# Kernel tuning notes

Hardware: AMD Instinct MI355X
Metric: run time of the kernel (lower is better)

Reference implementation:

```python
import jax, jax.numpy as jnp
import numpy as np

B, P, O, D, K, NREG, H, NLAYERS = 2, 2048, 512, 256, 3, 2, 8, 2
EPS_COS = 1e-8
EPS_LN = 1e-5


def setup_inputs() -> dict:
    key = jax.random.key(0)
    k = jax.random.split(key, 8)
    s = 0.02
    return {
        "x_path": jax.random.normal(k[0], (B, P, D), jnp.float32),
        "x_omic": jax.random.normal(k[1], (B, O, D), jnp.float32),
        "bottle_tokens": jax.random.uniform(k[2], (1, NREG, D), jnp.float32),
        "Wlp": jax.random.normal(k[3], (D, D), jnp.float32) * s,
        "blp": jnp.zeros((D,), jnp.float32),
        "Wlo": jax.random.normal(k[4], (D, D), jnp.float32) * s,
        "blo": jnp.zeros((D,), jnp.float32),
        "ln_g": jnp.ones((NLAYERS, D), jnp.float32),
        "ln_b": jnp.zeros((NLAYERS, D), jnp.float32),
        "Wqkv": jax.random.normal(k[5], (NLAYERS, D, 3 * D), jnp.float32) * s,
        "bqkv": jnp.zeros((NLAYERS, 3 * D), jnp.float32),
        "Wo": jax.random.normal(k[6], (NLAYERS, D, D), jnp.float32) * s,
        "bo": jnp.zeros((NLAYERS, D), jnp.float32),
    }


def _cosine_sim(xp, xo):
    # xp: [P, D], xo: [O, D] -> [P, O]; torch cosine_similarity semantics
    np_ = jnp.maximum(jnp.linalg.norm(xp, axis=-1), EPS_COS)
    no_ = jnp.maximum(jnp.linalg.norm(xo, axis=-1), EPS_COS)
    return (xp @ xo.T) / (np_[:, None] * no_[None, :])


def _greedy_pairs(sim):
    # exclusive greedy top-K matching == iterative argmax with row/col masking
    Pn, On = sim.shape

    def step(carry, _):
        rm, cm = carry
        masked = jnp.where(rm[:, None] | cm[None, :], -jnp.inf, sim)
        idx = jnp.argmax(masked)
        ip, io = idx // On, idx % On
        return (rm.at[ip].set(True), cm.at[io].set(True)), (ip, io)

    (rm, cm), (ips, ios) = jax.lax.scan(
        step, (jnp.zeros(Pn, bool), jnp.zeros(On, bool)), None, length=K)
    return ips, ios, rm, cm


def _remaining(x, mask, n_keep):
    # non-selected tokens in ascending original order (stable argsort)
    order = jnp.argsort(mask.astype(jnp.int32))
    return x[order[:n_keep]]


def _assemble_one(xp, xo, bottle, Wlp, blp, Wlo, blo):
    sim = _cosine_sim(xp, xo)  # indices are data-dependent but non-differentiable
    ips, ios, rm, cm = _greedy_pairs(sim)
    ks = (xp[ips] @ Wlp + blp) + (xo[ios] @ Wlo + blo)  # [K, D], in greedy order
    rem_p = _remaining(xp, rm, P - K)  # [P-K, D]
    rem_o = _remaining(xo, cm, O - K)  # [O-K, D]
    return jnp.concatenate([ks, rem_p, bottle, rem_o], axis=0)  # [L, D]


def _layernorm(x, g, b):
    mu = jnp.mean(x, axis=-1, keepdims=True)
    var = jnp.mean(jnp.square(x - mu), axis=-1, keepdims=True)
    return (x - mu) * jax.lax.rsqrt(var + EPS_LN) * g + b


def _mhsa(x, Wqkv, bqkv, Wo, bo):
    Bn, L, Dn = x.shape
    dh = Dn // H
    qkv = x @ Wqkv + bqkv  # [B, L, 3D]
    q, k, v = jnp.split(qkv, 3, axis=-1)
    q = q.reshape(Bn, L, H, dh)
    k = k.reshape(Bn, L, H, dh)
    v = v.reshape(Bn, L, H, dh)
    scores = jnp.einsum('bqhd,bkhd->bhqk', q, k) * (1.0 / np.sqrt(dh)).astype(x.dtype)
    attn = jax.nn.softmax(scores, axis=-1)
    out = jnp.einsum('bhqk,bkhd->bqhd', attn, v).reshape(Bn, L, Dn)
    return out @ Wo + bo


def reference(x_path, x_omic, bottle_tokens, Wlp, blp, Wlo, blo,
              ln_g, ln_b, Wqkv, bqkv, Wo, bo):
    path_len, token_len = P, NREG
    x = jax.vmap(_assemble_one, in_axes=(0, 0, None, None, None, None, None))(
        x_path, x_omic, bottle_tokens[0], Wlp, blp, Wlo, blo)  # [B, L, D]
    for l in range(NLAYERS):  # pre-LN residual attention block (TransLayer)
        x = x + _mhsa(_layernorm(x, ln_g[l], ln_b[l]), Wqkv[l], bqkv[l], Wo[l], bo[l])
    t_path, xp_out = x[:, :1, :], x[:, 1:path_len, :]
    t_omic = x[:, path_len + token_len:path_len + token_len + 1, :]
    xo_out = x[:, path_len + token_len + 1:, :]
    return (t_path, xp_out, t_omic, xo_out)
```

## Files before the change

kernel.cpp:

```cpp
#include <hip/hip_runtime.h>
#include <hip/hip_bf16.h>
#include <math.h>

namespace {
constexpr int Bn = 2, Pn = 2048, On = 512, Dn = 256, Kn = 3, NREG = 2, Hn = 8, NL = 2;
constexpr int Ln = Pn + NREG + On - Kn;
constexpr int Lpad = 2560;
constexpr int DH = 32;
constexpr int BH = Bn * Hn;
constexpr float EPS_COS = 1e-8f, EPS_LN = 1e-5f;
constexpr float QS2 = 0.17677669529663687f * 1.4426950408889634f;

using bf16x8 = __attribute__((ext_vector_type(8))) short;
using f32x4  = __attribute__((ext_vector_type(4))) float;

union U8 { int4 i4; ushort u[8]; short s[8]; bf16x8 b; };
union U4 { uint2 i2; ushort u[4]; };

__device__ inline ushort f2bf(float f) {
  union { __bf16 h; ushort u; } c; c.h = (__bf16)f; return c.u;
}

__device__ inline float fexp2(float x) {
#if __has_builtin(__builtin_amdgcn_exp2f)
  return __builtin_amdgcn_exp2f(x);
#else
  float r;
  asm("v_exp_f32 %0, %1" : "=v"(r) : "v"(x));
  return r;
#endif
}

__device__ inline int kswz(int r) {
  return ((r & 1) | ((r & 4) >> 1) | ((r & 2) << 1)) << 3;
}

template<int C> __device__ inline float dppf(float x) {
  return __builtin_bit_cast(float,
      __builtin_amdgcn_update_dpp(0, __builtin_bit_cast(int, x), C, 0xF, 0xF, false));
}
__device__ inline float red16_sum(float x) {
  x += dppf<0xB1>(x);
  x += dppf<0x4E>(x);
  x += dppf<0x124>(x);
  x += dppf<0x128>(x);
  return x;
}

__global__ void k_rownorm(const float* __restrict__ xp, const float* __restrict__ xo,
                          float* __restrict__ xps, float* __restrict__ xos) {
  int r = blockIdx.x;
  const float* src; float* dst;
  if (r < Bn * Pn) { src = xp + (size_t)r * Dn; dst = xps + (size_t)r * Dn; }
  else { int r2 = r - Bn * Pn; src = xo + (size_t)r2 * Dn; dst = xos + (size_t)r2 * Dn; }
  int tid = threadIdx.x;
  float v = src[tid];
  float ss = v * v;
  #pragma unroll
  for (int m = 32; m >= 1; m >>= 1) ss += __shfl_xor(ss, m, 64);
  __shared__ float wsum[4];
  if ((tid & 63) == 0) wsum[tid >> 6] = ss;
  __syncthreads();
  float tot = wsum[0] + wsum[1] + wsum[2] + wsum[3];
  dst[tid] = v * (1.f / fmaxf(sqrtf(tot), EPS_COS));
}

__global__ void k_transpose(const float* __restrict__ xos, float* __restrict__ xosT) {
  __shared__ float t[16][17];
  int b = blockIdx.z;
  int o0 = blockIdx.x * 16, d0 = blockIdx.y * 16;
  int tx = threadIdx.x & 15, ty = threadIdx.x >> 4;
  t[ty][tx] = xos[((size_t)b * On + o0 + ty) * Dn + d0 + tx];
  __syncthreads();
  xosT[((size_t)b * Dn + d0 + ty) * On + o0 + tx] = t[tx][ty];
}

__global__ void k_wprep(const float* __restrict__ W, ushort* __restrict__ Wt, int Kd, int N) {
  const int z = blockIdx.z;
  const int n0 = blockIdx.x * 16, k0 = blockIdx.y * 16;
  const int tx = threadIdx.x & 15, ty = threadIdx.x >> 4;
  __shared__ float t[16][17];
  t[ty][tx] = W[(size_t)z * Kd * N + (size_t)(k0 + ty) * N + n0 + tx];
  __syncthreads();
  Wt[(size_t)z * Kd * N + (size_t)(n0 + ty) * Kd + k0 + tx] = f2bf(t[tx][ty]);
}

__global__ __launch_bounds__(256) void k_gemm64(
    const float* __restrict__ A, long sA,
    const float* __restrict__ Wm, long sW,
    float* __restrict__ C, long sC,
    int M, int N, int Kd)
{
  const int bz = blockIdx.z;
  A += (size_t)bz * sA; Wm += (size_t)bz * sW; C += (size_t)bz * sC;
  const int bm = blockIdx.x * 64, bn = blockIdx.y * 64;
  __shared__ __attribute__((aligned(16))) float As[64][33];
  __shared__ __attribute__((aligned(16))) float Bs[32][64];
  const int tid = threadIdx.x;
  const int ty = tid >> 4, tx = tid & 15;
  const int arow = tid >> 3, acol = (tid & 7) * 4;
  const int brow = tid >> 4, bcol = (tid & 15) * 4;
  float acc[4][4] = {};
  for (int k0 = 0; k0 < Kd; k0 += 32) {
    __syncthreads();
    #pragma unroll
    for (int pp = 0; pp < 2; ++pp) {
      int r = arow + pp * 32;
      float4 v = *(const float4*)(A + (size_t)(bm + r) * Kd + k0 + acol);
      As[r][acol + 0] = v.x; As[r][acol + 1] = v.y; As[r][acol + 2] = v.z; As[r][acol + 3] = v.w;
      int r2 = brow + pp * 16;
      *(float4*)&Bs[r2][bcol] = *(const float4*)(Wm + (size_t)(k0 + r2) * N + bn + bcol);
    }
    __syncthreads();
    #pragma unroll
    for (int kk = 0; kk < 32; ++kk) {
      float a0 = As[ty * 4 + 0][kk], a1 = As[ty * 4 + 1][kk];
      float a2 = As[ty * 4 + 2][kk], a3 = As[ty * 4 + 3][kk];
      float4 bq = *(const float4*)&Bs[kk][tx * 4];
      acc[0][0] += a0 * bq.x; acc[0][1] += a0 * bq.y; acc[0][2] += a0 * bq.z; acc[0][3] += a0 * bq.w;
      acc[1][0] += a1 * bq.x; acc[1][1] += a1 * bq.y; acc[1][2] += a1 * bq.z; acc[1][3] += a1 * bq.w;
      acc[2][0] += a2 * bq.x; acc[2][1] += a2 * bq.y; acc[2][2] += a2 * bq.z; acc[2][3] += a2 * bq.w;
      acc[3][0] += a3 * bq.x; acc[3][1] += a3 * bq.y; acc[3][2] += a3 * bq.z; acc[3][3] += a3 * bq.w;
    }
  }
  #pragma unroll
  for (int i = 0; i < 4; ++i) {
    int gr = bm + ty * 4 + i;
    *(float4*)(C + (size_t)gr * N + bn + tx * 4) =
        make_float4(acc[i][0], acc[i][1], acc[i][2], acc[i][3]);
  }
}

__global__ __launch_bounds__(64) void k_gemm_qkv(
    const ushort* __restrict__ A, const ushort* __restrict__ Bt,
    const float* __restrict__ bias,
    ushort* __restrict__ Qh, ushort* __restrict__ Kh, ushort* __restrict__ Vtg, int M)
{
  const int m0 = blockIdx.x * 64, n0 = blockIdx.y * 64;
  const int lane = threadIdx.x, lm = lane & 15, lh = lane >> 4;
  f32x4 acc[4][4] = {};
  int rA[4];
  #pragma unroll
  for (int mi = 0; mi < 4; ++mi) { int r = m0 + mi * 16 + lm; rA[mi] = r < M ? r : M - 1; }
  const ushort* bp0 = Bt + (size_t)(n0 +  0 + lm) * 256 + lh * 8;
  const ushort* bp1 = Bt + (size_t)(n0 + 16 + lm) * 256 + lh * 8;
  const ushort* bp2 = Bt + (size_t)(n0 + 32 + lm) * 256 + lh * 8;
  const ushort* bp3 = Bt + (size_t)(n0 + 48 + lm) * 256 + lh * 8;
  #pragma unroll
  for (int k0 = 0; k0 < 256; k0 += 32) {
    U8 a0, a1, a2, a3, b0, b1, b2, b3;
    a0.i4 = *(const int4*)(A + (size_t)rA[0] * 256 + k0 + lh * 8);
    a1.i4 = *(const int4*)(A + (size_t)rA[1] * 256 + k0 + lh * 8);
    a2.i4 = *(const int4*)(A + (size_t)rA[2] * 256 + k0 + lh * 8);
    a3.i4 = *(const int4*)(A + (size_t)rA[3] * 256 + k0 + lh * 8);
    b0.i4 = *(const int4*)(bp0 + k0);
    b1.i4 = *(const int4*)(bp1 + k0);
    b2.i4 = *(const int4*)(bp2 + k0);
    b3.i4 = *(const int4*)(bp3 + k0);
    acc[0][0] = __builtin_amdgcn_mfma_f32_16x16x32_bf16(a0.b, b0.b, acc[0][0], 0, 0, 0);
    acc[0][1] = __builtin_amdgcn_mfma_f32_16x16x32_bf16(a0.b, b1.b, acc[0][1], 0, 0, 0);
    acc[0][2] = __builtin_amdgcn_mfma_f32_16x16x32_bf16(a0.b, b2.b, acc[0][2], 0, 0, 0);
    acc[0][3] = __builtin_amdgcn_mfma_f32_16x16x32_bf16(a0.b, b3.b, acc[0][3], 0, 0, 0);
    acc[1][0] = __builtin_amdgcn_mfma_f32_16x16x32_bf16(a1.b, b0.b, acc[1][0], 0, 0, 0);
    acc[1][1] = __builtin_amdgcn_mfma_f32_16x16x32_bf16(a1.b, b1.b, acc[1][1], 0, 0, 0);
    acc[1][2] = __builtin_amdgcn_mfma_f32_16x16x32_bf16(a1.b, b2.b, acc[1][2], 0, 0, 0);
    acc[1][3] = __builtin_amdgcn_mfma_f32_16x16x32_bf16(a1.b, b3.b, acc[1][3], 0, 0, 0);
    acc[2][0] = __builtin_amdgcn_mfma_f32_16x16x32_bf16(a2.b, b0.b, acc[2][0], 0, 0, 0);
    acc[2][1] = __builtin_amdgcn_mfma_f32_16x16x32_bf16(a2.b, b1.b, acc[2][1], 0, 0, 0);
    acc[2][2] = __builtin_amdgcn_mfma_f32_16x16x32_bf16(a2.b, b2.b, acc[2][2], 0, 0, 0);
    acc[2][3] = __builtin_amdgcn_mfma_f32_16x16x32_bf16(a2.b, b3.b, acc[2][3], 0, 0, 0);
    acc[3][0] = __builtin_amdgcn_mfma_f32_16x16x32_bf16(a3.b, b0.b, acc[3][0], 0, 0, 0);
    acc[3][1] = __builtin_amdgcn_mfma_f32_16x16x32_bf16(a3.b, b1.b, acc[3][1], 0, 0, 0);
    acc[3][2] = __builtin_amdgcn_mfma_f32_16x16x32_bf16(a3.b, b2.b, acc[3][2], 0, 0, 0);
    acc[3][3] = __builtin_amdgcn_mfma_f32_16x16x32_bf16(a3.b, b3.b, acc[3][3], 0, 0, 0);
  }
  const int typ = n0 >> 8;
  #pragma unroll
  for (int g = 0; g < 4; ++g) {
    const int hh = ((n0 & 255) + 16 * g) >> 5;
    const int dcol = (16 * g + lm) & 31;
    const float bv = bias[n0 + 16 * g + lm];
    #pragma unroll
    for (int mi = 0; mi < 4; ++mi) {
      #pragma unroll
      for (int i = 0; i < 4; ++i) {
        int row = m0 + mi * 16 + lh * 4 + i;
        if (row >= M) continue;
        int b = (row >= Ln) ? 1 : 0;
        int t = row - b * Ln;
        float v = acc[mi][g][i] + bv;
        size_t bhh = (size_t)(b * Hn + hh);
        if (typ == 0) {
          Qh[(bhh * Lpad + t) * 32 + dcol] = f2bf(v * QS2);
        } else if (typ == 1) {
          Kh[(bhh * Lpad + t) * 32 + dcol] = f2bf(v);
        } else {
          int tp = (t & ~63) | ((t & 15) << 2) | ((t >> 4) & 3);
          Vtg[bhh * (size_t)(32 * Lpad) + (size_t)dcol * Lpad + tp] = f2bf(v);
        }
      }
    }
  }
}

template<bool LAST>
__global__ __launch_bounds__(64) void k_gemm_out(
    const ushort* __restrict__ A, const ushort* __restrict__ Bt,
    const float* __restrict__ bias, const float* __restrict__ resid,
    float* __restrict__ C, float* __restrict__ outp, int M, int N)
{
  const int m0 = blockIdx.x * 64, n0 = blockIdx.y * 32;
  const int lane = threadIdx.x, lm = lane & 15, lh = lane >> 4;
  f32x4 acc[4][2] = {};
  int rA[4];
  #pragma unroll
  for (int mi = 0; mi < 4; ++mi) { int r = m0 + mi * 16 + lm; rA[mi] = r < M ? r : M - 1; }
  const ushort* bp0 = Bt + (size_t)(n0 + lm) * 256 + lh * 8;
  const ushort* bp1 = Bt + (size_t)(n0 + 16 + lm) * 256 + lh * 8;
  #pragma unroll
  for (int k0 = 0; k0 < 256; k0 += 32) {
    U8 a0, a1, a2, a3, bb0, bb1;
    a0.i4 = *(const int4*)(A + (size_t)rA[0] * 256 + k0 + lh * 8);
    a1.i4 = *(const int4*)(A + (size_t)rA[1] * 256 + k0 + lh * 8);
    a2.i4 = *(const int4*)(A + (size_t)rA[2] * 256 + k0 + lh * 8);
    a3.i4 = *(const int4*)(A + (size_t)rA[3] * 256 + k0 + lh * 8);
    bb0.i4 = *(const int4*)(bp0 + k0);
    bb1.i4 = *(const int4*)(bp1 + k0);
    acc[0][0] = __builtin_amdgcn_mfma_f32_16x16x32_bf16(a0.b, bb0.b, acc[0][0], 0, 0, 0);
    acc[0][1] = __builtin_amdgcn_mfma_f32_16x16x32_bf16(a0.b, bb1.b, acc[0][1], 0, 0, 0);
    acc[1][0] = __builtin_amdgcn_mfma_f32_16x16x32_bf16(a1.b, bb0.b, acc[1][0], 0, 0, 0);
    acc[1][1] = __builtin_amdgcn_mfma_f32_16x16x32_bf16(a1.b, bb1.b, acc[1][1], 0, 0, 0);
    acc[2][0] = __builtin_amdgcn_mfma_f32_16x16x32_bf16(a2.b, bb0.b, acc[2][0], 0, 0, 0);
    acc[2][1] = __builtin_amdgcn_mfma_f32_16x16x32_bf16(a2.b, bb1.b, acc[2][1], 0, 0, 0);
    acc[3][0] = __builtin_amdgcn_mfma_f32_16x16x32_bf16(a3.b, bb0.b, acc[3][0], 0, 0, 0);
    acc[3][1] = __builtin_amdgcn_mfma_f32_16x16x32_bf16(a3.b, bb1.b, acc[3][1], 0, 0, 0);
  }
  const float bv0 = bias[n0 + lm], bv1 = bias[n0 + 16 + lm];
  #pragma unroll
  for (int mi = 0; mi < 4; ++mi) {
    #pragma unroll
    for (int i = 0; i < 4; ++i) {
      int row = m0 + mi * 16 + lh * 4 + i;
      if (row >= M) continue;
      float v0 = acc[mi][0][i] + bv0 + resid[(size_t)row * N + n0 + lm];
      float v1 = acc[mi][1][i] + bv1 + resid[(size_t)row * N + n0 + 16 + lm];
      if (!LAST) {
        C[(size_t)row * N + n0 + lm] = v0;
        C[(size_t)row * N + n0 + 16 + lm] = v1;
      } else {
        int b = (row >= Ln) ? 1 : 0;
        int t = row - b * Ln;
        size_t off;
        if (t == 0) off = (size_t)b * Dn;
        else if (t < Pn) off = (size_t)Bn * Dn + ((size_t)b * (Pn - 1) + (t - 1)) * Dn;
        else if (t < Pn + NREG) continue;
        else if (t == Pn + NREG) off = (size_t)Bn * Dn + (size_t)Bn * (Pn - 1) * Dn + (size_t)b * Dn;
        else off = (size_t)Bn * Dn * 2 + (size_t)Bn * (Pn - 1) * Dn +
                   ((size_t)b * (On - Kn - 1) + (t - (Pn + NREG + 1))) * Dn;
        outp[off + n0 + lm] = v0;
        outp[off + n0 + 16 + lm] = v1;
      }
    }
  }
}

__global__ __launch_bounds__(64) void k_top3(const float* __restrict__ sim,
                                             float* __restrict__ t3v, int* __restrict__ t3c) {
  const int row = blockIdx.x, lane = threadIdx.x;
  const float* rp = sim + (size_t)row * On + lane * 8;
  float4 va = *(const float4*)rp, vb2 = *(const float4*)(rp + 4);
  float v[8] = { va.x, va.y, va.z, va.w, vb2.x, vb2.y, vb2.z, vb2.w };
  int ex = 0;
  for (int s = 0; s < 3; ++s) {
    float bv = -INFINITY; int bi = 1 << 30;
    #pragma unroll
    for (int j = 0; j < 8; ++j) {
      int idx = lane * 8 + j;
      bool ok = !((ex >> j) & 1);
      if (ok && (v[j] > bv || (v[j] == bv && idx < bi))) { bv = v[j]; bi = idx; }
    }
    #pragma unroll
    for (int m = 1; m < 64; m <<= 1) {
      float ov = __shfl_xor(bv, m, 64); int oi = __shfl_xor(bi, m, 64);
      if (ov > bv || (ov == bv && oi < bi)) { bv = ov; bi = oi; }
    }
    if (lane == 0) { t3v[(size_t)row * 3 + s] = bv; t3c[(size_t)row * 3 + s] = bi; }
    if ((bi >> 3) == lane) ex |= 1 << (bi & 7);
  }
}

__global__ __launch_bounds__(1024) void k_greedy(const float* __restrict__ t3v,
                                                 const int* __restrict__ t3c, int* __restrict__ sel) {
  const int b = blockIdx.x, tid = threadIdx.x;
  __shared__ float redv[1024];
  __shared__ long long redi[1024];
  __shared__ int selp[3], selc[3];
  const float* tv = t3v + (size_t)b * Pn * 3;
  const int*   tc = t3c + (size_t)b * Pn * 3;
  for (int s = 0; s < 3; ++s) {
    float bvv = -INFINITY; long long bi = 0x7fffffffffffffffLL;
    for (int p = tid; p < Pn; p += 1024) {
      bool used = false;
      for (int u = 0; u < s; ++u) used |= (selp[u] == p);
      if (used) continue;
      #pragma unroll
      for (int j = 0; j < 3; ++j) {
        int cc = tc[p * 3 + j];
        bool cused = false;
        for (int u = 0; u < s; ++u) cused |= (selc[u] == cc);
        if (cused) continue;
        float vv = tv[p * 3 + j];
        long long fi = (long long)p * On + cc;
        if (vv > bvv || (vv == bvv && fi < bi)) { bvv = vv; bi = fi; }
      }
    }
    redv[tid] = bvv; redi[tid] = bi;
    __syncthreads();
    for (int off = 512; off; off >>= 1) {
      if (tid < off) {
        if (redv[tid + off] > redv[tid] ||
            (redv[tid + off] == redv[tid] && redi[tid + off] < redi[tid])) {
          redv[tid] = redv[tid + off]; redi[tid] = redi[tid + off];
        }
      }
      __syncthreads();
    }
    if (tid == 0) { selp[s] = (int)(redi[0] / On); selc[s] = (int)(redi[0] % On); }
    __syncthreads();
  }
  if (tid == 0) {
    int* o = sel + b * 12;
    int sp0 = selp[0], sp1 = selp[1], sp2 = selp[2];
    int sc0 = selc[0], sc1 = selc[1], sc2 = selc[2];
    o[0] = sp0; o[1] = sp1; o[2] = sp2; o[3] = sc0; o[4] = sc1; o[5] = sc2;
    int t;
    if (sp0 > sp1) { t = sp0; sp0 = sp1; sp1 = t; }
    if (sp1 > sp2) { t = sp1; sp1 = sp2; sp2 = t; }
    if (sp0 > sp1) { t = sp0; sp0 = sp1; sp1 = t; }
    if (sc0 > sc1) { t = sc0; sc0 = sc1; sc1 = t; }
    if (sc1 > sc2) { t = sc1; sc1 = sc2; sc2 = t; }
    if (sc0 > sc1) { t = sc0; sc0 = sc1; sc1 = t; }
    o[6] = sp0; o[7] = sp1; o[8] = sp2; o[9] = sc0; o[10] = sc1; o[11] = sc2;
  }
}

__device__ inline void ln_write(float v, const float* __restrict__ g,
                                const float* __restrict__ bb, ushort* __restrict__ dst,
                                int tid) {
  float s = v;
  #pragma unroll
  for (int m = 32; m >= 1; m >>= 1) s += __shfl_xor(s, m, 64);
  __shared__ float w1[4], w2[4];
  if ((tid & 63) == 0) w1[tid >> 6] = s;
  __syncthreads();
  float mu = (w1[0] + w1[1] + w1[2] + w1[3]) * (1.f / Dn);
  float d = v - mu;
  float q = d * d;
  #pragma unroll
  for (int m = 32; m >= 1; m >>= 1) q += __shfl_xor(q, m, 64);
  if ((tid & 63) == 0) w2[tid >> 6] = q;
  __syncthreads();
  float var = (w2[0] + w2[1] + w2[2] + w2[3]) * (1.f / Dn);
  dst[tid] = f2bf(d * rsqrtf(var + EPS_LN) * g[tid] + bb[tid]);
}

__global__ void k_pair_ln(const float* __restrict__ xp, const float* __restrict__ xo,
                          const float* __restrict__ Wlp, const float* __restrict__ blp,
                          const float* __restrict__ Wlo, const float* __restrict__ blo,
                          const int* __restrict__ sel, const float* __restrict__ g,
                          const float* __restrict__ bb,
                          float* __restrict__ x, ushort* __restrict__ xnb) {
  const int k = blockIdx.x, b = blockIdx.y, d = threadIdx.x;
  const int ip = sel[b * 12 + k], io = sel[b * 12 + 3 + k];
  const float* xpr = xp + ((size_t)b * Pn + ip) * Dn;
  const float* xom = xo + ((size_t)b * On + io) * Dn;
  float acc = blp[d] + blo[d];
  for (int i = 0; i < Dn; ++i)
    acc += xpr[i] * Wlp[(size_t)i * Dn + d] + xom[i] * Wlo[(size_t)i * Dn + d];
  const size_t row = (size_t)b * Ln + k;
  x[row * Dn + d] = acc;
  ln_write(acc, g, bb, xnb + row * Dn, d);
}

__global__ void k_gather_ln(const float* __restrict__ xp, const float* __restrict__ xo,
                            const float* __restrict__ bottle, const int* __restrict__ sel,
                            const float* __restrict__ g, const float* __restrict__ bb,
                            float* __restrict__ x, ushort* __restrict__ xnb) {
  const int idx = blockIdx.x;
  const int b = idx / Ln, t = idx % Ln;
  if (t < Kn) return;
  const float* src;
  if (t < Pn) {
    const int* rp = sel + b * 12 + 6;
    int s2 = t - Kn;
    if (s2 >= rp[0]) s2++;
    if (s2 >= rp[1]) s2++;
    if (s2 >= rp[2]) s2++;
    src = xp + ((size_t)b * Pn + s2) * Dn;
  } else if (t < Pn + NREG) {
    src = bottle + (size_t)(t - Pn) * Dn;
  } else {
    const int* ro = sel + b * 12 + 9;
    int s2 = t - (Pn + NREG);
    if (s2 >= ro[0]) s2++;
    if (s2 >= ro[1]) s2++;
    if (s2 >= ro[2]) s2++;
    src = xo + ((size_t)b * On + s2) * Dn;
  }
  float v = src[threadIdx.x];
  x[(size_t)idx * Dn + threadIdx.x] = v;
  ln_write(v, g, bb, xnb + (size_t)idx * Dn, threadIdx.x);
}

__global__ void k_ln(const float* __restrict__ x, const float* __restrict__ g,
                     const float* __restrict__ bb, ushort* __restrict__ xnb) {
  const size_t row = blockIdx.x;
  const int tid = threadIdx.x;
  ln_write(x[row * Dn + tid], g, bb, xnb + row * Dn, tid);
}

__global__ __launch_bounds__(128) void k_flash_mfma(const ushort* __restrict__ Qh,
                                                    const ushort* __restrict__ Kh,
                                                    const ushort* __restrict__ Vtg,
                                                    float* __restrict__ Opart,
                                                    float* __restrict__ lpart) {
  const int qt = blockIdx.x, h = blockIdx.y;
  const int bz = blockIdx.z, b = bz >> 1, sp = bz & 1;
  const int q0 = qt * 32;
  const int tid = threadIdx.x;
  const int w = tid >> 6, lane = tid & 63;
  const int lm = lane & 15, lh = lane >> 4;
  __shared__ __attribute__((aligned(16))) short Ks[64 * 64];
  __shared__ __attribute__((aligned(16))) short Vt[32 * 64];
  __shared__ __attribute__((aligned(16))) short Ps[2][1024];
  const int bh = b * Hn + h;
  const ushort* Qg = Qh + (size_t)bh * Lpad * 32;
  const ushort* Kg = Kh + (size_t)bh * Lpad * 32 + (size_t)sp * 1280 * 32;
  const ushort* Vg = Vtg + (size_t)bh * (32 * Lpad) + (size_t)sp * 1280;
  U8 aq;
  aq.i4 = *(const int4*)(Qg + (size_t)(q0 + w * 16 + lm) * 32 + lh * 8);
  float lsum[4] = {0.f, 0.f, 0.f, 0.f};
  f32x4 O0 = {0.f, 0.f, 0.f, 0.f}, O1 = {0.f, 0.f, 0.f, 0.f};
  const f32x4 zacc = {0.f, 0.f, 0.f, 0.f};
  const int key2 = tid >> 1, khalf = (tid & 1) * 16;
  const int vd = tid >> 2, vseg = (tid & 3) * 16;
  const ushort* kbase = Kg + (size_t)key2 * 32 + khalf;
  const ushort* vbase = Vg + (size_t)vd * Lpad + vseg;
  const int kw1 = (key2 * 64 + khalf) ^ kswz(key2);
  const int kw2 = (key2 * 64 + khalf + 8) ^ kswz(key2);
  const int vw1 = (vd * 64 + vseg) ^ kswz(vd);
  const int vw2 = (vd * 64 + vseg + 8) ^ kswz(vd);
  const int NTL = 20;
  int4 ka = ((const int4*)kbase)[0], kb2 = ((const int4*)kbase)[1];
  int4 va = ((const int4*)vbase)[0], vb2 = ((const int4*)vbase)[1];
  for (int kt = 0; kt < NTL; ++kt) {
    const int k0 = kt * 64;
    __syncthreads();
    *(int4*)&Ks[kw1] = ka;
    *(int4*)&Ks[kw2] = kb2;
    *(int4*)&Vt[vw1] = va;
    *(int4*)&Vt[vw2] = vb2;
    if (kt + 1 < NTL) {
      const int4* ks = (const int4*)(kbase + (size_t)(k0 + 64) * 32);
      ka = ks[0]; kb2 = ks[1];
      const int4* vs = (const int4*)(vbase + k0 + 64);
      va = vs[0]; vb2 = vs[1];
    }
    __syncthreads();
    U8 b0, b1, b2, b3;
    const int ksw = kswz(lm);
    b0.i4 = *(const int4*)&Ks[(( 0 + lm) * 64 + lh * 8) ^ ksw];
    b1.i4 = *(const int4*)&Ks[((16 + lm) * 64 + lh * 8) ^ ksw];
    b2.i4 = *(const int4*)&Ks[((32 + lm) * 64 + lh * 8) ^ ksw];
    b3.i4 = *(const int4*)&Ks[((48 + lm) * 64 + lh * 8) ^ ksw];
    f32x4 S0 = __builtin_amdgcn_mfma_f32_16x16x32_bf16(aq.b, b0.b, zacc, 0, 0, 0);
    f32x4 S1 = __builtin_amdgcn_mfma_f32_16x16x32_bf16(aq.b, b1.b, zacc, 0, 0, 0);
    f32x4 S2 = __builtin_amdgcn_mfma_f32_16x16x32_bf16(aq.b, b2.b, zacc, 0, 0, 0);
    f32x4 S3 = __builtin_amdgcn_mfma_f32_16x16x32_bf16(aq.b, b3.b, zacc, 0, 0, 0);
    const int kg = sp * 1280 + k0;
    const bool tail = (kg + 64 > Ln);
    #pragma unroll
    for (int i = 0; i < 4; ++i) {
      float v0 = S0[i], v1 = S1[i], v2 = S2[i], v3 = S3[i];
      if (tail) {
        v0 = (kg +  0 + lm < Ln) ? v0 : -INFINITY;
        v1 = (kg + 16 + lm < Ln) ? v1 : -INFINITY;
        v2 = (kg + 32 + lm < Ln) ? v2 : -INFINITY;
        v3 = (kg + 48 + lm < Ln) ? v3 : -INFINITY;
      }
      float p0 = fexp2(v0), p1 = fexp2(v1);
      float p2 = fexp2(v2), p3 = fexp2(v3);
      lsum[i] += (p0 + p1) + (p2 + p3);
      U4 pw;
      pw.u[0] = f2bf(p0); pw.u[1] = f2bf(p1); pw.u[2] = f2bf(p2); pw.u[3] = f2bf(p3);
      const int r = lh * 4 + i;
      const int idxw = (r * 64 + lm * 4) ^ ((r & 7) << 3);
      *(uint2*)&Ps[w][idxw] = pw.i2;
    }
    U8 pa0, pa1, v00, v01, v10, v11;
    {
      const int ra = lm * 64, sw = (lm & 7) << 3;
      pa0.i4 = *(const int4*)&Ps[w][(ra +      lh * 8) ^ sw];
      pa1.i4 = *(const int4*)&Ps[w][(ra + 32 + lh * 8) ^ sw];
    }
    {
      const int vsw = kswz(lm);
      v00.i4 = *(const int4*)&Vt[((     lm) * 64 +      lh * 8) ^ vsw];
      v01.i4 = *(const int4*)&Vt[((16 + lm) * 64 +      lh * 8) ^ vsw];
      v10.i4 = *(const int4*)&Vt[((     lm) * 64 + 32 + lh * 8) ^ vsw];
      v11.i4 = *(const int4*)&Vt[((16 + lm) * 64 + 32 + lh * 8) ^ vsw];
    }
    O0 = __builtin_amdgcn_mfma_f32_16x16x32_bf16(pa0.b, v00.b, O0, 0, 0, 0);
    O0 = __builtin_amdgcn_mfma_f32_16x16x32_bf16(pa1.b, v10.b, O0, 0, 0, 0);
    O1 = __builtin_amdgcn_mfma_f32_16x16x32_bf16(pa0.b, v01.b, O1, 0, 0, 0);
    O1 = __builtin_amdgcn_mfma_f32_16x16x32_bf16(pa1.b, v11.b, O1, 0, 0, 0);
  }
  #pragma unroll
  for (int i = 0; i < 4; ++i) {
    float lred = red16_sum(lsum[i]);
    int grow = q0 + w * 16 + lh * 4 + i;
    if (grow < Ln) {
      float* op = Opart + ((size_t)(sp * BH + bh) * Lpad + grow) * 32;
      op[lm]      = O0[i];
      op[16 + lm] = O1[i];
      if (lm == 0) lpart[(size_t)(sp * BH + bh) * Lpad + grow] = lred;
    }
  }
}

__global__ __launch_bounds__(256) void k_combine(const float* __restrict__ Opart,
                                                 const float* __restrict__ lpart,
                                                 ushort* __restrict__ attnb) {
  const int idx = blockIdx.x * 256 + threadIdx.x;
  const int d = idx & 31;
  const int rest = idx >> 5;
  const int bh = rest / Ln;
  const int q = rest - bh * Ln;
  const float o = Opart[((size_t)bh * Lpad + q) * 32 + d] +
                  Opart[((size_t)(BH + bh) * Lpad + q) * 32 + d];
  const float l = lpart[(size_t)bh * Lpad + q] +
                  lpart[(size_t)(BH + bh) * Lpad + q];
  const int b = bh >> 3, h = bh & 7;
  attnb[((size_t)b * Ln + q) * Dn + h * 32 + d] = f2bf(o / l);
}

}

extern "C" void kernel_launch(void* const* d_in, const int* in_sizes, int n_in,
                              void* d_out, int out_size, void* d_ws, size_t ws_size,
                              hipStream_t stream) {
  const float* x_path = (const float*)d_in[0];
  const float* x_omic = (const float*)d_in[1];
  const float* bottle = (const float*)d_in[2];
  const float* Wlp    = (const float*)d_in[3];
  const float* blp    = (const float*)d_in[4];
  const float* Wlo    = (const float*)d_in[5];
  const float* blo    = (const float*)d_in[6];
  const float* ln_g   = (const float*)d_in[7];
  const float* ln_b   = (const float*)d_in[8];
  const float* Wqkv   = (const float*)d_in[9];
  const float* bqkv   = (const float*)d_in[10];
  const float* Wo     = (const float*)d_in[11];
  const float* bo     = (const float*)d_in[12];
  float* out = (float*)d_out;

  char* base = (char*)d_ws;
  auto alloc = [&](size_t bytes) { char* p = base; base += (bytes + 255) & ~(size_t)255; return p; };
  int*    sel    = (int*)alloc(256);
  float*  x      = (float*)alloc(sizeof(float) * Bn * Ln * Dn);
  ushort* xnb    = (ushort*)alloc(sizeof(ushort) * Bn * Ln * Dn);
  ushort* attnb  = (ushort*)alloc(sizeof(ushort) * Bn * Ln * Dn);
  ushort* Qh     = (ushort*)alloc(sizeof(ushort) * Bn * Hn * Lpad * 32);
  ushort* Kh     = (ushort*)alloc(sizeof(ushort) * Bn * Hn * Lpad * 32);
  ushort* Vtg    = (ushort*)alloc(sizeof(ushort) * Bn * Hn * 32 * Lpad);
  ushort* WqkvT  = (ushort*)alloc(sizeof(ushort) * NL * Dn * 3 * Dn);
  ushort* WoT    = (ushort*)alloc(sizeof(ushort) * NL * Dn * Dn);
  float*  xps    = (float*)alloc(sizeof(float) * Bn * Pn * Dn);
  float*  xos    = (float*)alloc(sizeof(float) * Bn * On * Dn);
  float*  xosT   = (float*)alloc(sizeof(float) * Bn * On * Dn);
  float*  simb   = (float*)alloc(sizeof(float) * Bn * Pn * On);
  float*  t3v    = (float*)alloc(sizeof(float) * Bn * Pn * 3);
  int*    t3c    = (int*)alloc(sizeof(int) * Bn * Pn * 3);
  float* Opart = xps;
  float* lpart = xps + (size_t)2 * BH * Lpad * 32;

  k_wprep<<<dim3(768 / 16, 256 / 16, NL), 256, 0, stream>>>(Wqkv, WqkvT, 256, 768);
  k_wprep<<<dim3(256 / 16, 256 / 16, NL), 256, 0, stream>>>(Wo, WoT, 256, 256);

  k_rownorm<<<Bn * (Pn + On), 256, 0, stream>>>(x_path, x_omic, xps, xos);
  k_transpose<<<dim3(On / 16, Dn / 16, Bn), 256, 0, stream>>>(xos, xosT);
  k_gemm64<<<dim3(Pn / 64, On / 64, Bn), 256, 0, stream>>>(
      xps, (long)Pn * Dn, xosT, (long)Dn * On, simb, (long)Pn * On, Pn, On, Dn);
  k_top3<<<Bn * Pn, 64, 0, stream>>>(simb, t3v, t3c);
  k_greedy<<<Bn, 1024, 0, stream>>>(t3v, t3c, sel);
  k_pair_ln<<<dim3(Kn, Bn), 256, 0, stream>>>(x_path, x_omic, Wlp, blp, Wlo, blo, sel,
                                              ln_g, ln_b, x, xnb);
  k_gather_ln<<<Bn * Ln, 256, 0, stream>>>(x_path, x_omic, bottle, sel, ln_g, ln_b, x, xnb);

  const int Mrows = Bn * Ln;
  const int cgrid = (BH * Ln * 32) / 256;
  k_gemm_qkv<<<dim3(80, 12), 64, 0, stream>>>(xnb, WqkvT, bqkv, Qh, Kh, Vtg, Mrows);
  k_flash_mfma<<<dim3(80, Hn, Bn * 2), 128, 0, stream>>>(Qh, Kh, Vtg, Opart, lpart);
  k_combine<<<cgrid, 256, 0, stream>>>(Opart, lpart, attnb);
  k_gemm_out<false><<<dim3(80, 8), 64, 0, stream>>>(attnb, WoT, bo, x, x, nullptr, Mrows, Dn);
  k_ln<<<Mrows, 256, 0, stream>>>(x, ln_g + Dn, ln_b + Dn, xnb);
  k_gemm_qkv<<<dim3(80, 12), 64, 0, stream>>>(xnb, WqkvT + (size_t)Dn * 3 * Dn,
                                              bqkv + 3 * Dn, Qh, Kh, Vtg, Mrows);
  k_flash_mfma<<<dim3(80, Hn, Bn * 2), 128, 0, stream>>>(Qh, Kh, Vtg, Opart, lpart);
  k_combine<<<cgrid, 256, 0, stream>>>(Opart, lpart, attnb);
  k_gemm_out<true><<<dim3(80, 8), 64, 0, stream>>>(attnb, WoT + (size_t)Dn * Dn,
                                                   bo + Dn, x, nullptr, out, Mrows, Dn);
}
```

Measured before the change: 306.1 us.

## Compute cosine-sim on MFMA with split-bf16 operands and shrink GEMM row tiles

Replaces the fp32 SIMT similarity GEMM and the separate transpose with an MFMA kernel. Row-normalized inputs are split into bf16 high and low parts and three bf16 products are summed to keep near-fp32 accuracy for the greedy argmax. The QKV and output-projection GEMMs move from 64-row to 32-row tiles, which doubles the number of blocks for better CU occupancy. Opart/lpart now get their own workspace buffers instead of aliasing xps. The split-bf16 products may still change near-tie argmax picks compared with fp32.

Result: faster. 289.9 us (-5.3%).

```diff
diff --git a/kernel.cpp b/kernel.cpp
--- a/kernel.cpp
+++ b/kernel.cpp
@@ -20,6 +20,9 @@
 __device__ inline ushort f2bf(float f) {
   union { __bf16 h; ushort u; } c; c.h = (__bf16)f; return c.u;
 }
+__device__ inline float bf2f(ushort u) {
+  union { unsigned u; float f; } c; c.u = (unsigned)u << 16; return c.f;
+}
 
 __device__ inline float fexp2(float x) {
 #if __has_builtin(__builtin_amdgcn_exp2f)
@@ -48,11 +51,16 @@
 }
 
 __global__ void k_rownorm(const float* __restrict__ xp, const float* __restrict__ xo,
-                          float* __restrict__ xps, float* __restrict__ xos) {
+                          ushort* __restrict__ xph, ushort* __restrict__ xpl,
+                          ushort* __restrict__ xoh, ushort* __restrict__ xol) {
   int r = blockIdx.x;
-  const float* src; float* dst;
-  if (r < Bn * Pn) { src = xp + (size_t)r * Dn; dst = xps + (size_t)r * Dn; }
-  else { int r2 = r - Bn * Pn; src = xo + (size_t)r2 * Dn; dst = xos + (size_t)r2 * Dn; }
+  const float* src; ushort* dh; ushort* dl;
+  if (r < Bn * Pn) {
+    src = xp + (size_t)r * Dn; dh = xph + (size_t)r * Dn; dl = xpl + (size_t)r * Dn;
+  } else {
+    int r2 = r - Bn * Pn;
+    src = xo + (size_t)r2 * Dn; dh = xoh + (size_t)r2 * Dn; dl = xol + (size_t)r2 * Dn;
+  }
   int tid = threadIdx.x;
   float v = src[tid];
   float ss = v * v;
@@ -62,17 +70,64 @@
   if ((tid & 63) == 0) wsum[tid >> 6] = ss;
   __syncthreads();
   float tot = wsum[0] + wsum[1] + wsum[2] + wsum[3];
-  dst[tid] = v * (1.f / fmaxf(sqrtf(tot), EPS_COS));
-}
-
-__global__ void k_transpose(const float* __restrict__ xos, float* __restrict__ xosT) {
-  __shared__ float t[16][17];
-  int b = blockIdx.z;
-  int o0 = blockIdx.x * 16, d0 = blockIdx.y * 16;
-  int tx = threadIdx.x & 15, ty = threadIdx.x >> 4;
-  t[ty][tx] = xos[((size_t)b * On + o0 + ty) * Dn + d0 + tx];
-  __syncthreads();
-  xosT[((size_t)b * Dn + d0 + ty) * On + o0 + tx] = t[tx][ty];
+  float val = v * (1.f / fmaxf(sqrtf(tot), EPS_COS));
+  ushort hi = f2bf(val);
+  dh[tid] = hi;
+  dl[tid] = f2bf(val - bf2f(hi));
+}
+
+__global__ __launch_bounds__(64) void k_sim(
+    const ushort* __restrict__ Ah, const ushort* __restrict__ Al,
+    const ushort* __restrict__ Bh, const ushort* __restrict__ Bl,
+    float* __restrict__ C)
+{
+  const int b = blockIdx.z;
+  const int m0 = blockIdx.x * 32, n0 = blockIdx.y * 32;
+  const int lane = threadIdx.x, lm = lane & 15, lh = lane >> 4;
+  const ushort* ah = Ah + (size_t)b * Pn * 256;
+  const ushort* al = Al + (size_t)b * Pn * 256;
+  const ushort* bh = Bh + (size_t)b * On * 256;
+  const ushort* bl = Bl + (size_t)b * On * 256;
+  const size_t a0off = (size_t)(m0 + lm) * 256 + lh * 8;
+  const size_t a1off = (size_t)(m0 + 16 + lm) * 256 + lh * 8;
+  const size_t b0off = (size_t)(n0 + lm) * 256 + lh * 8;
+  const size_t b1off = (size_t)(n0 + 16 + lm) * 256 + lh * 8;
+  f32x4 acc[2][2] = {};
+  #pragma unroll
+  for (int k0 = 0; k0 < 256; k0 += 32) {
+    U8 a0h, a0l, a1h, a1l, b0h, b0l, b1h, b1l;
+    a0h.i4 = *(const int4*)(ah + a0off + k0);
+    a0l.i4 = *(const int4*)(al + a0off + k0);
+    a1h.i4 = *(const int4*)(ah + a1off + k0);
+    a1l.i4 = *(const int4*)(al + a1off + k0);
+    b0h.i4 = *(const int4*)(bh + b0off + k0);
+    b0l.i4 = *(const int4*)(bl + b0off + k0);
+    b1h.i4 = *(const int4*)(bh + b1off + k0);
+    b1l.i4 = *(const int4*)(bl + b1off + k0);
+    acc[0][0] = __builtin_amdgcn_mfma_f32_16x16x32_bf16(a0h.b, b0h.b, acc[0][0], 0, 0, 0);
+    acc[0][1] = __builtin_amdgcn_mfma_f32_16x16x32_bf16(a0h.b, b1h.b, acc[0][1], 0, 0, 0);
+    acc[1][0] = __builtin_amdgcn_mfma_f32_16x16x32_bf16(a1h.b, b0h.b, acc[1][0], 0, 0, 0);
+    acc[1][1] = __builtin_amdgcn_mfma_f32_16x16x32_bf16(a1h.b, b1h.b, acc[1][1], 0, 0, 0);
+    acc[0][0] = __builtin_amdgcn_mfma_f32_16x16x32_bf16(a0h.b, b0l.b, acc[0][0], 0, 0, 0);
+    acc[0][1] = __builtin_amdgcn_mfma_f32_16x16x32_bf16(a0h.b, b1l.b, acc[0][1], 0, 0, 0);
+    acc[1][0] = __builtin_amdgcn_mfma_f32_16x16x32_bf16(a1h.b, b0l.b, acc[1][0], 0, 0, 0);
+    acc[1][1] = __builtin_amdgcn_mfma_f32_16x16x32_bf16(a1h.b, b1l.b, acc[1][1], 0, 0, 0);
+    acc[0][0] = __builtin_amdgcn_mfma_f32_16x16x32_bf16(a0l.b, b0h.b, acc[0][0], 0, 0, 0);
+    acc[0][1] = __builtin_amdgcn_mfma_f32_16x16x32_bf16(a0l.b, b1h.b, acc[0][1], 0, 0, 0);
+    acc[1][0] = __builtin_amdgcn_mfma_f32_16x16x32_bf16(a1l.b, b0h.b, acc[1][0], 0, 0, 0);
+    acc[1][1] = __builtin_amdgcn_mfma_f32_16x16x32_bf16(a1l.b, b1h.b, acc[1][1], 0, 0, 0);
+  }
+  float* Cb = C + (size_t)b * Pn * On;
+  #pragma unroll
+  for (int mi = 0; mi < 2; ++mi) {
+    #pragma unroll
+    for (int i = 0; i < 4; ++i) {
+      int row = m0 + mi * 16 + lh * 4 + i;
+      #pragma unroll
+      for (int ni = 0; ni < 2; ++ni)
+        Cb[(size_t)row * On + n0 + ni * 16 + lm] = acc[mi][ni][i];
+    }
+  }
 }
 
 __global__ void k_wprep(const float* __restrict__ W, ushort* __restrict__ Wt, int Kd, int N) {
@@ -85,74 +140,26 @@
   Wt[(size_t)z * Kd * N + (size_t)(n0 + ty) * Kd + k0 + tx] = f2bf(t[tx][ty]);
 }
 
-__global__ __launch_bounds__(256) void k_gemm64(
-    const float* __restrict__ A, long sA,
-    const float* __restrict__ Wm, long sW,
-    float* __restrict__ C, long sC,
-    int M, int N, int Kd)
-{
-  const int bz = blockIdx.z;
-  A += (size_t)bz * sA; Wm += (size_t)bz * sW; C += (size_t)bz * sC;
-  const int bm = blockIdx.x * 64, bn = blockIdx.y * 64;
-  __shared__ __attribute__((aligned(16))) float As[64][33];
-  __shared__ __attribute__((aligned(16))) float Bs[32][64];
-  const int tid = threadIdx.x;
-  const int ty = tid >> 4, tx = tid & 15;
-  const int arow = tid >> 3, acol = (tid & 7) * 4;
-  const int brow = tid >> 4, bcol = (tid & 15) * 4;
-  float acc[4][4] = {};
-  for (int k0 = 0; k0 < Kd; k0 += 32) {
-    __syncthreads();
-    #pragma unroll
-    for (int pp = 0; pp < 2; ++pp) {
-      int r = arow + pp * 32;
-      float4 v = *(const float4*)(A + (size_t)(bm + r) * Kd + k0 + acol);
-      As[r][acol + 0] = v.x; As[r][acol + 1] = v.y; As[r][acol + 2] = v.z; As[r][acol + 3] = v.w;
-      int r2 = brow + pp * 16;
-      *(float4*)&Bs[r2][bcol] = *(const float4*)(Wm + (size_t)(k0 + r2) * N + bn + bcol);
-    }
-    __syncthreads();
-    #pragma unroll
-    for (int kk = 0; kk < 32; ++kk) {
-      float a0 = As[ty * 4 + 0][kk], a1 = As[ty * 4 + 1][kk];
-      float a2 = As[ty * 4 + 2][kk], a3 = As[ty * 4 + 3][kk];
-      float4 bq = *(const float4*)&Bs[kk][tx * 4];
-      acc[0][0] += a0 * bq.x; acc[0][1] += a0 * bq.y; acc[0][2] += a0 * bq.z; acc[0][3] += a0 * bq.w;
-      acc[1][0] += a1 * bq.x; acc[1][1] += a1 * bq.y; acc[1][2] += a1 * bq.z; acc[1][3] += a1 * bq.w;
-      acc[2][0] += a2 * bq.x; acc[2][1] += a2 * bq.y; acc[2][2] += a2 * bq.z; acc[2][3] += a2 * bq.w;
-      acc[3][0] += a3 * bq.x; acc[3][1] += a3 * bq.y; acc[3][2] += a3 * bq.z; acc[3][3] += a3 * bq.w;
-    }
-  }
-  #pragma unroll
-  for (int i = 0; i < 4; ++i) {
-    int gr = bm + ty * 4 + i;
-    *(float4*)(C + (size_t)gr * N + bn + tx * 4) =
-        make_float4(acc[i][0], acc[i][1], acc[i][2], acc[i][3]);
-  }
-}
-
 __global__ __launch_bounds__(64) void k_gemm_qkv(
     const ushort* __restrict__ A, const ushort* __restrict__ Bt,
     const float* __restrict__ bias,
     ushort* __restrict__ Qh, ushort* __restrict__ Kh, ushort* __restrict__ Vtg, int M)
 {
-  const int m0 = blockIdx.x * 64, n0 = blockIdx.y * 64;
+  const int m0 = blockIdx.x * 32, n0 = blockIdx.y * 64;
   const int lane = threadIdx.x, lm = lane & 15, lh = lane >> 4;
-  f32x4 acc[4][4] = {};
-  int rA[4];
-  #pragma unroll
-  for (int mi = 0; mi < 4; ++mi) { int r = m0 + mi * 16 + lm; rA[mi] = r < M ? r : M - 1; }
+  f32x4 acc[2][4] = {};
+  int rA[2];
+  #pragma unroll
+  for (int mi = 0; mi < 2; ++mi) { int r = m0 + mi * 16 + lm; rA[mi] = r < M ? r : M - 1; }
   const ushort* bp0 = Bt + (size_t)(n0 +  0 + lm) * 256 + lh * 8;
   const ushort* bp1 = Bt + (size_t)(n0 + 16 + lm) * 256 + lh * 8;
   const ushort* bp2 = Bt + (size_t)(n0 + 32 + lm) * 256 + lh * 8;
   const ushort* bp3 = Bt + (size_t)(n0 + 48 + lm) * 256 + lh * 8;
   #pragma unroll
   for (int k0 = 0; k0 < 256; k0 += 32) {
-    U8 a0, a1, a2, a3, b0, b1, b2, b3;
+    U8 a0, a1, b0, b1, b2, b3;
     a0.i4 = *(const int4*)(A + (size_t)rA[0] * 256 + k0 + lh * 8);
     a1.i4 = *(const int4*)(A + (size_t)rA[1] * 256 + k0 + lh * 8);
-    a2.i4 = *(const int4*)(A + (size_t)rA[2] * 256 + k0 + lh * 8);
-    a3.i4 = *(const int4*)(A + (size_t)rA[3] * 256 + k0 + lh * 8);
     b0.i4 = *(const int4*)(bp0 + k0);
     b1.i4 = *(const int4*)(bp1 + k0);
     b2.i4 = *(const int4*)(bp2 + k0);
@@ -165,14 +172,6 @@
     acc[1][1] = __builtin_amdgcn_mfma_f32_16x16x32_bf16(a1.b, b1.b, acc[1][1], 0, 0, 0);
     acc[1][2] = __builtin_amdgcn_mfma_f32_16x16x32_bf16(a1.b, b2.b, acc[1][2], 0, 0, 0);
     acc[1][3] = __builtin_amdgcn_mfma_f32_16x16x32_bf16(a1.b, b3.b, acc[1][3], 0, 0, 0);
-    acc[2][0] = __builtin_amdgcn_mfma_f32_16x16x32_bf16(a2.b, b0.b, acc[2][0], 0, 0, 0);
-    acc[2][1] = __builtin_amdgcn_mfma_f32_16x16x32_bf16(a2.b, b1.b, acc[2][1], 0, 0, 0);
-    acc[2][2] = __builtin_amdgcn_mfma_f32_16x16x32_bf16(a2.b, b2.b, acc[2][2], 0, 0, 0);
-    acc[2][3] = __builtin_amdgcn_mfma_f32_16x16x32_bf16(a2.b, b3.b, acc[2][3], 0, 0, 0);
-    acc[3][0] = __builtin_amdgcn_mfma_f32_16x16x32_bf16(a3.b, b0.b, acc[3][0], 0, 0, 0);
-    acc[3][1] = __builtin_amdgcn_mfma_f32_16x16x32_bf16(a3.b, b1.b, acc[3][1], 0, 0, 0);
-    acc[3][2] = __builtin_amdgcn_mfma_f32_16x16x32_bf16(a3.b, b2.b, acc[3][2], 0, 0, 0);
-    acc[3][3] = __builtin_amdgcn_mfma_f32_16x16x32_bf16(a3.b, b3.b, acc[3][3], 0, 0, 0);
   }
   const int typ = n0 >> 8;
   #pragma unroll
@@ -181,7 +180,7 @@
     const int dcol = (16 * g + lm) & 31;
     const float bv = bias[n0 + 16 * g + lm];
     #pragma unroll
-    for (int mi = 0; mi < 4; ++mi) {
+    for (int mi = 0; mi < 2; ++mi) {
       #pragma unroll
       for (int i = 0; i < 4; ++i) {
         int row = m0 + mi * 16 + lh * 4 + i;
@@ -209,35 +208,29 @@
     const float* __restrict__ bias, const float* __restrict__ resid,
     float* __restrict__ C, float* __restrict__ outp, int M, int N)
 {
-  const int m0 = blockIdx.x * 64, n0 = blockIdx.y * 32;
+  const int m0 = blockIdx.x * 32, n0 = blockIdx.y * 32;
   const int lane = threadIdx.x, lm = lane & 15, lh = lane >> 4;
-  f32x4 acc[4][2] = {};
-  int rA[4];
-  #pragma unroll
-  for (int mi = 0; mi < 4; ++mi) { int r = m0 + mi * 16 + lm; rA[mi] = r < M ? r : M - 1; }
+  f32x4 acc[2][2] = {};
+  int rA[2];
+  #pragma unroll
+  for (int mi = 0; mi < 2; ++mi) { int r = m0 + mi * 16 + lm; rA[mi] = r < M ? r : M - 1; }
   const ushort* bp0 = Bt + (size_t)(n0 + lm) * 256 + lh * 8;
   const ushort* bp1 = Bt + (size_t)(n0 + 16 + lm) * 256 + lh * 8;
   #pragma unroll
   for (int k0 = 0; k0 < 256; k0 += 32) {
-    U8 a0, a1, a2, a3, bb0, bb1;
+    U8 a0, a1, bb0, bb1;
     a0.i4 = *(const int4*)(A + (size_t)rA[0] * 256 + k0 + lh * 8);
     a1.i4 = *(const int4*)(A + (size_t)rA[1] * 256 + k0 + lh * 8);
-    a2.i4 = *(const int4*)(A + (size_t)rA[2] * 256 + k0 + lh * 8);
-    a3.i4 = *(const int4*)(A + (size_t)rA[3] * 256 + k0 + lh * 8);
     bb0.i4 = *(const int4*)(bp0 + k0);
     bb1.i4 = *(const int4*)(bp1 + k0);
     acc[0][0] = __builtin_amdgcn_mfma_f32_16x16x32_bf16(a0.b, bb0.b, acc[0][0], 0, 0, 0);
     acc[0][1] = __builtin_amdgcn_mfma_f32_16x16x32_bf16(a0.b, bb1.b, acc[0][1], 0, 0, 0);
     acc[1][0] = __builtin_amdgcn_mfma_f32_16x16x32_bf16(a1.b, bb0.b, acc[1][0], 0, 0, 0);
     acc[1][1] = __builtin_amdgcn_mfma_f32_16x16x32_bf16(a1.b, bb1.b, acc[1][1], 0, 0, 0);
-    acc[2][0] = __builtin_amdgcn_mfma_f32_16x16x32_bf16(a2.b, bb0.b, acc[2][0], 0, 0, 0);
-    acc[2][1] = __builtin_amdgcn_mfma_f32_16x16x32_bf16(a2.b, bb1.b, acc[2][1], 0, 0, 0);
-    acc[3][0] = __builtin_amdgcn_mfma_f32_16x16x32_bf16(a3.b, bb0.b, acc[3][0], 0, 0, 0);
-    acc[3][1] = __builtin_amdgcn_mfma_f32_16x16x32_bf16(a3.b, bb1.b, acc[3][1], 0, 0, 0);
   }
   const float bv0 = bias[n0 + lm], bv1 = bias[n0 + 16 + lm];
   #pragma unroll
-  for (int mi = 0; mi < 4; ++mi) {
+  for (int mi = 0; mi < 2; ++mi) {
     #pragma unroll
     for (int i = 0; i < 4; ++i) {
       int row = m0 + mi * 16 + lh * 4 + i;
@@ -575,22 +568,21 @@
   ushort* Vtg    = (ushort*)alloc(sizeof(ushort) * Bn * Hn * 32 * Lpad);
   ushort* WqkvT  = (ushort*)alloc(sizeof(ushort) * NL * Dn * 3 * Dn);
   ushort* WoT    = (ushort*)alloc(sizeof(ushort) * NL * Dn * Dn);
-  float*  xps    = (float*)alloc(sizeof(float) * Bn * Pn * Dn);
-  float*  xos    = (float*)alloc(sizeof(float) * Bn * On * Dn);
-  float*  xosT   = (float*)alloc(sizeof(float) * Bn * On * Dn);
+  ushort* xph    = (ushort*)alloc(sizeof(ushort) * Bn * Pn * Dn);
+  ushort* xpl    = (ushort*)alloc(sizeof(ushort) * Bn * Pn * Dn);
+  ushort* xoh    = (ushort*)alloc(sizeof(ushort) * Bn * On * Dn);
+  ushort* xol    = (ushort*)alloc(sizeof(ushort) * Bn * On * Dn);
   float*  simb   = (float*)alloc(sizeof(float) * Bn * Pn * On);
   float*  t3v    = (float*)alloc(sizeof(float) * Bn * Pn * 3);
   int*    t3c    = (int*)alloc(sizeof(int) * Bn * Pn * 3);
-  float* Opart = xps;
-  float* lpart = xps + (size_t)2 * BH * Lpad * 32;
+  float*  Opart  = (float*)alloc(sizeof(float) * 2 * BH * Lpad * 32);
+  float*  lpart  = (float*)alloc(sizeof(float) * 2 * BH * Lpad);
 
   k_wprep<<<dim3(768 / 16, 256 / 16, NL), 256, 0, stream>>>(Wqkv, WqkvT, 256, 768);
   k_wprep<<<dim3(256 / 16, 256 / 16, NL), 256, 0, stream>>>(Wo, WoT, 256, 256);
 
-  k_rownorm<<<Bn * (Pn + On), 256, 0, stream>>>(x_path, x_omic, xps, xos);
-  k_transpose<<<dim3(On / 16, Dn / 16, Bn), 256, 0, stream>>>(xos, xosT);
-  k_gemm64<<<dim3(Pn / 64, On / 64, Bn), 256, 0, stream>>>(
-      xps, (long)Pn * Dn, xosT, (long)Dn * On, simb, (long)Pn * On, Pn, On, Dn);
+  k_rownorm<<<Bn * (Pn + On), 256, 0, stream>>>(x_path, x_omic, xph, xpl, xoh, xol);
+  k_sim<<<dim3(Pn / 32, On / 32, Bn), 64, 0, stream>>>(xph, xpl, xoh, xol, simb);
   k_top3<<<Bn * Pn, 64, 0, stream>>>(simb, t3v, t3c);
   k_greedy<<<Bn, 1024, 0, stream>>>(t3v, t3c, sel);
   k_pair_ln<<<dim3(Kn, Bn), 256, 0, stream>>>(x_path, x_omic, Wlp, blp, Wlo, blo, sel,
@@ -598,16 +590,17 @@
   k_gather_ln<<<Bn * Ln, 256, 0, stream>>>(x_path, x_omic, bottle, sel, ln_g, ln_b, x, xnb);
 
   const int Mrows = Bn * Ln;
+  const int mt32 = (Mrows + 31) / 32;
   const int cgrid = (BH * Ln * 32) / 256;
-  k_gemm_qkv<<<dim3(80, 12), 64, 0, stream>>>(xnb, WqkvT, bqkv, Qh, Kh, Vtg, Mrows);
+  k_gemm_qkv<<<dim3(mt32, 12), 64, 0, stream>>>(xnb, WqkvT, bqkv, Qh, Kh, Vtg, Mrows);
   k_flash_mfma<<<dim3(80, Hn, Bn * 2), 128, 0, stream>>>(Qh, Kh, Vtg, Opart, lpart);
   k_combine<<<cgrid, 256, 0, stream>>>(Opart, lpart, attnb);
-  k_gemm_out<false><<<dim3(80, 8), 64, 0, stream>>>(attnb, WoT, bo, x, x, nullptr, Mrows, Dn);
+  k_gemm_out<false><<<dim3(mt32, 8), 64, 0, stream>>>(attnb, WoT, bo, x, x, nullptr, Mrows, Dn);
   k_ln<<<Mrows, 256, 0, stream>>>(x, ln_g + Dn, ln_b + Dn, xnb);
-  k_gemm_qkv<<<dim3(80, 12), 64, 0, stream>>>(xnb, WqkvT + (size_t)Dn * 3 * Dn,
-                                              bqkv + 3 * Dn, Qh, Kh, Vtg, Mrows);
+  k_gemm_qkv<<<dim3(mt32, 12), 64, 0, stream>>>(xnb, WqkvT + (size_t)Dn * 3 * Dn,
+                                                bqkv + 3 * Dn, Qh, Kh, Vtg, Mrows);
   k_flash_mfma<<<dim3(80, Hn, Bn * 2), 128, 0, stream>>>(Qh, Kh, Vtg, Opart, lpart);
   k_combine<<<cgrid, 256, 0, stream>>>(Opart, lpart, attnb);
-  k_gemm_out<true><<<dim3(80, 8), 64, 0, stream>>>(attnb, WoT + (size_t)Dn * Dn,
-                                                   bo + Dn, x, nullptr, out, Mrows, Dn);
-}
+  k_gemm_out<true><<<dim3(mt32, 8), 64, 0, stream>>>(attnb, WoT + (size_t)Dn * Dn,
+                                                     bo + Dn, x, nullptr, out, Mrows, Dn);
+}
```
